# Performance work log

Measured on AMD Instinct MI355X. Metric: run time of the kernel, lower is better.

Reference implementation:

```python
import jax, jax.numpy as jnp
import numpy as np
import math

DIM = 2048
NH = 16
Q_RANK = 1536
KV_RANK = 512
D_NOPE = 128
D_ROPE = 64
D_V = 128
EPS = 1e-6
B, S = 2, 2048
THETA = 10000.0


def _rms_norm(x, w):
    return x * jax.lax.rsqrt(jnp.mean(x * x, axis=-1, keepdims=True) + EPS) * w


def _rope_cos_sin(seq_len, d):
    inv_freq = 1.0 / (THETA ** (jnp.arange(0, d, 2, dtype=jnp.float32) / d))
    t = jnp.arange(seq_len, dtype=jnp.float32)
    freqs = jnp.outer(t, inv_freq)  # (s, d/2)
    return jnp.cos(freqs), jnp.sin(freqs)


def _apply_rope(x, cos, sin):
    # x: (b, s, h, d), rotate interleaved pairs (llama-style complex rotation)
    x1 = x[..., 0::2]
    x2 = x[..., 1::2]
    c = cos[None, :, None, :]
    s = sin[None, :, None, :]
    o1 = x1 * c - x2 * s
    o2 = x1 * s + x2 * c
    return jnp.stack([o1, o2], axis=-1).reshape(x.shape)


def setup_inputs() -> dict:
    key = jax.random.key(0)
    ks = jax.random.split(key, 10)
    sd = 0.02
    return {
        "x": jax.random.normal(ks[0], (B, S, DIM), dtype=jnp.float32),
        # torch nn.Linear weights: (out_features, in_features), y = x @ W.T
        "wq_down": jax.random.normal(ks[1], (Q_RANK, DIM), dtype=jnp.float32) * sd,
        "wq_up": jax.random.normal(ks[2], (NH * D_NOPE, Q_RANK), dtype=jnp.float32) * sd,
        "wq_rope": jax.random.normal(ks[3], (NH * D_ROPE, Q_RANK), dtype=jnp.float32) * sd,
        "q_norm_w": jnp.ones((Q_RANK,), dtype=jnp.float32),
        "wkv_down": jax.random.normal(ks[4], (KV_RANK, DIM), dtype=jnp.float32) * sd,
        "kv_norm_w": jnp.ones((KV_RANK,), dtype=jnp.float32),
        "wkv_up": jax.random.normal(ks[5], (NH * (D_NOPE + D_V), KV_RANK), dtype=jnp.float32) * sd,
        "wk_rope": jax.random.normal(ks[6], (D_ROPE, DIM), dtype=jnp.float32) * sd,
        "wo": jax.random.normal(ks[7], (DIM, NH * D_V), dtype=jnp.float32) * sd,
    }


def reference(x, wq_down, wq_up, wq_rope, q_norm_w, wkv_down, kv_norm_w, wkv_up, wk_rope, wo):
    bs, seq_len, _ = x.shape
    # --- Q low-rank path ---
    q_c = _rms_norm(x @ wq_down.T, q_norm_w)                    # (b, s, q_rank)
    q_nope = (q_c @ wq_up.T).reshape(bs, seq_len, NH, D_NOPE)
    q_pe = (q_c @ wq_rope.T).reshape(bs, seq_len, NH, D_ROPE)
    # --- KV low-rank path ---
    kv_c = _rms_norm(x @ wkv_down.T, kv_norm_w)                 # (b, s, kv_rank)
    kv_up = (kv_c @ wkv_up.T).reshape(bs, seq_len, NH, D_NOPE + D_V)
    k_nope = kv_up[..., :D_NOPE]
    v = kv_up[..., D_NOPE:]                                     # (b, s, h, dv)
    # shared single-head rope key
    k_rope_shared = (x @ wk_rope.T).reshape(bs, seq_len, 1, D_ROPE)
    # --- partial-dim RoPE ---
    cos, sin = _rope_cos_sin(seq_len, D_ROPE)
    q_pe = _apply_rope(q_pe, cos, sin)
    k_rope_shared = _apply_rope(k_rope_shared, cos, sin)
    k_rope = jnp.broadcast_to(k_rope_shared, (bs, seq_len, NH, D_ROPE))
    # --- concat nope + rope dims ---
    q = jnp.concatenate([q_nope, q_pe], axis=-1)                # (b, s, h, dn+dr)
    k = jnp.concatenate([k_nope, k_rope], axis=-1)
    scale = 1.0 / math.sqrt(D_NOPE + D_ROPE)
    scores = jnp.einsum("bqhd,bkhd->bhqk", q, k) * scale        # (b, h, s, s)
    causal = jnp.tril(jnp.ones((seq_len, seq_len), dtype=bool))
    scores = jnp.where(causal[None, None], scores, -jnp.inf)
    probs = jax.nn.softmax(scores.astype(jnp.float32), axis=-1).astype(q.dtype)
    out = jnp.einsum("bhqk,bkhd->bqhd", probs, v)               # (b, s, h, dv)
    out = out.reshape(bs, seq_len, NH * D_V)
    return out @ wo.T


if __name__ == "__main__":
    inp = setup_inputs()
    y = jax.jit(reference)(**inp)
    print(y.shape, y.dtype)
```

## Files before the change

kernel.cpp:

```cpp
#include <hip/hip_runtime.h>
#include <hip/hip_bf16.h>
#include <math.h>

#define NHH 16
#define SS  2048
#define TT  4096
#define DQK 192
#define QSCALE 0.07216878364870322f
#define ROPE_C 0.28782313662425574f

typedef __bf16 bf16x8 __attribute__((ext_vector_type(8)));
typedef float f32x4 __attribute__((ext_vector_type(4)));

#define GLOAD16(gp, lp) __builtin_amdgcn_global_load_lds( \
    (const __attribute__((address_space(1))) void*)(gp),  \
    (__attribute__((address_space(3))) void*)(lp), 16, 0, 0)

#define SEG0 8388608
#define SEG1 11534336
#define SEG2 12582912
#define SEG3 12713984
#define SEG4 15859712
#define SEG5 17432576
#define SEG6 19529728
#define SEG7 23724032

__global__ __launch_bounds__(256) void cast_all(
        const float* __restrict__ x, const float* __restrict__ wqd,
        const float* __restrict__ wkvd, const float* __restrict__ wkr,
        const float* __restrict__ wqu, const float* __restrict__ wqr,
        const float* __restrict__ wkvu, const float* __restrict__ wo,
        __bf16* __restrict__ xb, __bf16* __restrict__ wqd_b,
        __bf16* __restrict__ wkvd_b, __bf16* __restrict__ wkr_b,
        __bf16* __restrict__ wqu_b, __bf16* __restrict__ wqr_b,
        __bf16* __restrict__ wkvu_b, __bf16* __restrict__ wo_b) {
    const int i = (blockIdx.x * 256 + threadIdx.x) * 8;
    const float* src;
    __bf16* dst;
    int off;
    if (i < SEG0)      { src = x;    dst = xb;     off = i; }
    else if (i < SEG1) { src = wqd;  dst = wqd_b;  off = i - SEG0; }
    else if (i < SEG2) { src = wkvd; dst = wkvd_b; off = i - SEG1; }
    else if (i < SEG3) { src = wkr;  dst = wkr_b;  off = i - SEG2; }
    else if (i < SEG4) { src = wqu;  dst = wqu_b;  off = i - SEG3; }
    else if (i < SEG5) { src = wqr;  dst = wqr_b;  off = i - SEG4; }
    else if (i < SEG6) { src = wkvu; dst = wkvu_b; off = i - SEG5; }
    else               { src = wo;   dst = wo_b;   off = i - SEG6; }
    const float4 a = *(const float4*)(src + off);
    const float4 b = *(const float4*)(src + off + 4);
    __bf16 o[8] = {(__bf16)a.x, (__bf16)a.y, (__bf16)a.z, (__bf16)a.w,
                   (__bf16)b.x, (__bf16)b.y, (__bf16)b.z, (__bf16)b.w};
    *(bf16x8*)(dst + off) = *(const bf16x8*)o;
}

__global__ __launch_bounds__(256) void rmsnorm_k(const float* __restrict__ in,
                                                 __bf16* __restrict__ out,
                                                 const float* __restrict__ w, int N) {
    const int row = blockIdx.x;
    const float* xr = in + (size_t)row * N;
    float ss = 0.f;
    for (int i = threadIdx.x; i < N; i += 256) {
        float v = xr[i];
        ss += v * v;
    }
    __shared__ float red[256];
    red[threadIdx.x] = ss;
    __syncthreads();
    for (int s = 128; s > 0; s >>= 1) {
        if (threadIdx.x < s) red[threadIdx.x] += red[threadIdx.x + s];
        __syncthreads();
    }
    const float scale = rsqrtf(red[0] / (float)N + 1e-6f);
    __bf16* orow = out + (size_t)row * N;
    for (int i = threadIdx.x; i < N; i += 256) orow[i] = (__bf16)(xr[i] * scale * w[i]);
}

template<int MODE>
__global__ __launch_bounds__(512, 1) void gemm9(
        const __bf16* __restrict__ A,
        const __bf16* __restrict__ W0, const __bf16* __restrict__ W1,
        const __bf16* __restrict__ W2,
        float* __restrict__ F0, float* __restrict__ F1,
        __bf16* __restrict__ B0, __bf16* __restrict__ B1,
        int M, int N, int Kin) {
    __shared__ __bf16 lds[3 * 24576];
    const int tid = threadIdx.x;
    const int w = tid >> 6, l = tid & 63;
    const int lr = l & 15, lg = l >> 4;
    const int wm = w >> 2, wn = w & 3;

    int m0, n0, nlim = 256, K = Kin;
    bool isKV = false;
    const __bf16* Ause = A;
    if (MODE == 0) {
        const int fb = blockIdx.x;
        if (fb < 256) { m0 = (fb >> 3) * 128; n0 = (fb & 7) * 256; }
        else          { m0 = (fb - 256) * 128; n0 = 2048; }
        nlim = 2112 - n0;
    } else if (MODE == 1) {
        int fb = blockIdx.x;
        isKV = (fb >= 384);
        if (isKV) { fb -= 384; K = 512; Ause = (const __bf16*)F0; }
        m0 = (fb & 31) * 128;
        n0 = (fb >> 5) * 256;
    } else {
        m0 = blockIdx.y * 128; n0 = blockIdx.x * 256;
    }
    const bool fullB = (nlim >= 256);
    const bool wAct  = (wn * 64 < nlim);

    const int srow = (w << 3) + (l >> 3);
    const int scol = (l & 7) << 3;
    const int sswz = ((srow >> 1) & 7) << 3;
    const int csw  = scol ^ sswz;

    const __bf16* aptr[2];
#pragma unroll
    for (int a = 0; a < 2; ++a)
        aptr[a] = Ause + (size_t)(m0 + a * 64 + srow) * K + csw;

    const __bf16* bptr[4];
#pragma unroll
    for (int bb = 0; bb < 4; ++bb) {
        const int n = n0 + bb * 64 + srow;
        const __bf16* wp;
        if (MODE == 0) {
            if (n < 1536)      wp = W0 + (size_t)n * K;
            else if (n < 2048) wp = W1 + (size_t)(n - 1536) * K;
            else if (n < 2112) wp = W2 + (size_t)(n - 2048) * K;
            else               wp = W0;
        } else if (MODE == 1) {
            if (isKV)          wp = W2 + (size_t)n * K;
            else               wp = (n < 2048) ? W0 + (size_t)n * K
                                               : W1 + (size_t)(n - 2048) * K;
        } else {
            wp = W0 + (size_t)n * K;
        }
        bptr[bb] = wp + csw;
    }

    auto stA = [&](int t2, int a) {
        GLOAD16(aptr[a] + (size_t)t2 * 64,
                &lds[(t2 % 3) * 24576 + a * 4096 + tid * 8]);
    };
    auto stB = [&](int t2, int b) {
        GLOAD16(bptr[b] + (size_t)t2 * 64,
                &lds[(t2 % 3) * 24576 + 8192 + b * 4096 + tid * 8]);
    };

    const int rswz = ((lr >> 1) & 7) << 3;

    f32x4 acc[4][4];
#pragma unroll
    for (int i = 0; i < 4; ++i)
#pragma unroll
        for (int j = 0; j < 4; ++j) acc[i][j] = (f32x4){0.f, 0.f, 0.f, 0.f};

    const int NT = K >> 6;
#pragma unroll
    for (int t = 0; t < 2; ++t) {
        stA(t, 0); stA(t, 1);
        stB(t, 0);
        if (fullB) { stB(t, 1); stB(t, 2); stB(t, 3); }
    }

    for (int t = 0; t < NT; ++t) {
        if (t + 1 < NT) {
            if (fullB) asm volatile("s_waitcnt vmcnt(6)" ::: "memory");
            else       asm volatile("s_waitcnt vmcnt(3)" ::: "memory");
        } else {
            asm volatile("s_waitcnt vmcnt(0)" ::: "memory");
        }
        __builtin_amdgcn_s_barrier();

        const __bf16* As_ = &lds[(t % 3) * 24576];
        const __bf16* Bs_ = As_ + 8192;

        if (t + 2 < NT) {
            const int t2 = t + 2;
            stA(t2, 0); stA(t2, 1);
            stB(t2, 0);
            if (fullB) { stB(t2, 1); stB(t2, 2); stB(t2, 3); }
        }

        if (wAct) {
            bf16x8 fa[4][2], fb[4][2];
#pragma unroll
            for (int i = 0; i < 4; ++i)
#pragma unroll
                for (int kk = 0; kk < 2; ++kk)
                    fa[i][kk] = *(const bf16x8*)&As_[(wm * 64 + i * 16 + lr) * 64 +
                                                     ((kk * 32 + lg * 8) ^ rswz)];
#pragma unroll
            for (int j = 0; j < 4; ++j)
#pragma unroll
                for (int kk = 0; kk < 2; ++kk)
                    fb[j][kk] = *(const bf16x8*)&Bs_[(wn * 64 + j * 16 + lr) * 64 +
                                                     ((kk * 32 + lg * 8) ^ rswz)];
            __builtin_amdgcn_s_setprio(1);
#pragma unroll
            for (int i = 0; i < 4; ++i)
#pragma unroll
                for (int j = 0; j < 4; ++j)
#pragma unroll
                    for (int kk = 0; kk < 2; ++kk)
                        acc[i][j] = __builtin_amdgcn_mfma_f32_16x16x32_bf16(fa[i][kk], fb[j][kk], acc[i][j], 0, 0, 0);
            __builtin_amdgcn_s_setprio(0);
        }
    }

    if (!wAct) return;

#pragma unroll
    for (int i = 0; i < 4; ++i) {
#pragma unroll
        for (int j = 0; j < 4; ++j) {
#pragma unroll
            for (int r = 0; r < 4; ++r) {
                const int m = m0 + wm * 64 + i * 16 + lg * 4 + r;
                const int n = n0 + wn * 64 + j * 16 + lr;
                const float v = acc[i][j][r];
                float vp = 0.f;
                if (MODE == 0 || MODE == 1) vp = __shfl_xor(v, 1);
                if (MODE == 0) {
                    if (n < 1536) {
                        F0[(size_t)m * 1536 + n] = v;
                    } else if (n < 2048) {
                        F1[(size_t)m * 512 + (n - 1536)] = v;
                    } else if (n < 2112) {
                        const int jj = n - 2048;
                        const int fi = jj >> 1;
                        const int spos = m & (SS - 1);
                        const float freq = __expf(-ROPE_C * (float)fi);
                        const float ang = (float)spos * freq;
                        const float sn = __sinf(ang), cs = __cosf(ang);
                        const float o = (jj & 1) ? (vp * sn + v * cs) : (v * cs - vp * sn);
                        B0[(size_t)m * 64 + jj] = (__bf16)o;
                    }
                } else if (MODE == 1) {
                    if (!isKV) {
                        if (n < 2048) {
                            B0[(size_t)m * 3072 + (n >> 7) * 192 + (n & 127)] = (__bf16)(v * QSCALE);
                        } else {
                            const int jj = n - 2048;
                            const int h = jj >> 6, dd = jj & 63;
                            const int fi = dd >> 1;
                            const int spos = m & (SS - 1);
                            const float freq = __expf(-ROPE_C * (float)fi);
                            const float ang = (float)spos * freq;
                            const float sn = __sinf(ang), cs = __cosf(ang);
                            const float o = (dd & 1) ? (vp * sn + v * cs) : (v * cs - vp * sn);
                            B0[(size_t)m * 3072 + h * 192 + 128 + dd] = (__bf16)(o * QSCALE);
                        }
                    } else {
                        __bf16* vTo = (__bf16*)F1;
                        const int h = n >> 8, off = n & 255;
                        if (off < 128)
                            B1[(size_t)m * 2048 + h * 128 + off] = (__bf16)v;
                        else
                            vTo[(((size_t)(m >> 11) * NHH + h) * 128 + (off - 128)) * SS + (m & (SS - 1))] = (__bf16)v;
                    }
                } else {
                    F0[(size_t)m * N + n] = v;
                }
            }
        }
    }
}

__global__ __launch_bounds__(512, 1) void attn_mfma7(
        const __bf16* __restrict__ q, const __bf16* __restrict__ knope,
        const __bf16* __restrict__ krope, const __bf16* __restrict__ vT,
        __bf16* __restrict__ att) {
    const int flat = blockIdx.x;
    const int xcd = flat & 7;
    const int a0 = flat >> 3;
    const int bx = a0 & 7;
    const int g8 = ((a0 >> 3) << 3) | xcd;
    const int h = g8 & 15;
    const int b = g8 >> 4;

    const int tid = threadIdx.x;
    const int w  = tid >> 6;
    const int l  = tid & 63;
    const int lr = l & 15;
    const int lg = l >> 4;

    __shared__ __bf16 Ks[2][64][200];
    __shared__ __bf16 Vs[2][128][72];
    __shared__ __bf16 Ps[8][2][16][72];

    const int rg[2] = {bx * 128 + w * 16, (15 - bx) * 128 + w * 16};
    const int nkt = 2 * (15 - bx) + 2;

    bf16x8 sreg[5];
    auto stage_load = [&](int kv0) {
#pragma unroll
        for (int i = 0; i < 5; ++i) {
            const int gc = tid + 512 * i;
            if (gc < 1536) {
                const int row = gc / 24, cc = gc - row * 24;
                const size_t tt = (size_t)(b * SS + kv0 + row);
                const __bf16* src = (cc < 16)
                    ? knope + tt * 2048 + h * 128 + cc * 8
                    : krope + tt * 64 + (cc - 16) * 8;
                sreg[i] = *(const bf16x8*)src;
            } else {
                const int c = gc - 1536;
                const int row = c >> 3, cc = c & 7;
                sreg[i] = *(const bf16x8*)(vT + (((size_t)b * NHH + h) * 128 + row) * SS
                                              + kv0 + cc * 8);
            }
        }
    };
    auto stage_write = [&](int bi) {
#pragma unroll
        for (int i = 0; i < 5; ++i) {
            const int gc = tid + 512 * i;
            if (gc < 1536) {
                const int row = gc / 24, cc = gc - row * 24;
                *(bf16x8*)&Ks[bi][row][cc * 8] = sreg[i];
            } else {
                const int c = gc - 1536;
                *(bf16x8*)&Vs[bi][c >> 3][(c & 7) * 8] = sreg[i];
            }
        }
    };

    bf16x8 qf[2][6];
#pragma unroll
    for (int grp = 0; grp < 2; ++grp) {
        const __bf16* qb = q + (((size_t)(b * SS + rg[grp] + lr)) * NHH + h) * DQK + lg * 8;
#pragma unroll
        for (int c = 0; c < 6; ++c) qf[grp][c] = *(const bf16x8*)(qb + c * 32);
    }

    f32x4 O[2][8];
    float m_r[2][4], l_r[2][4];
#pragma unroll
    for (int grp = 0; grp < 2; ++grp) {
#pragma unroll
        for (int n = 0; n < 8; ++n) O[grp][n] = (f32x4){0.f, 0.f, 0.f, 0.f};
#pragma unroll
        for (int r = 0; r < 4; ++r) { m_r[grp][r] = -INFINITY; l_r[grp][r] = 0.f; }
    }

    stage_load(0);
    stage_write(0);
    __syncthreads();
    int cur = 0;

    for (int kt = 0; kt < nkt; ++kt) {
        const int kv0 = kt * 64;
        const bool hasNext = (kt + 1 < nkt);
        if (hasNext) stage_load(kv0 + 64);

        const bool act0 = kv0 <= rg[0] + 15;
        const bool act1 = kv0 <= rg[1] + 15;
        if (act1 || act0) {
            f32x4 sc[2][4];
#pragma unroll
            for (int s = 0; s < 4; ++s) {
                const int colb = kv0 + s * 16;
                if (colb <= rg[1] + 15 || colb <= rg[0] + 15) {
                    bf16x8 kf[6];
#pragma unroll
                    for (int c = 0; c < 6; ++c)
                        kf[c] = *(const bf16x8*)&Ks[cur][s * 16 + lr][c * 32 + lg * 8];
                    __builtin_amdgcn_s_setprio(1);
#pragma unroll
                    for (int grp = 0; grp < 2; ++grp) {
                        if (colb <= rg[grp] + 15) {
                            f32x4 acc = (f32x4){0.f, 0.f, 0.f, 0.f};
#pragma unroll
                            for (int c = 0; c < 6; ++c)
                                acc = __builtin_amdgcn_mfma_f32_16x16x32_bf16(qf[grp][c], kf[c], acc, 0, 0, 0);
                            sc[grp][s] = acc;
                        } else {
                            sc[grp][s] = (f32x4){-INFINITY, -INFINITY, -INFINITY, -INFINITY};
                        }
                    }
                    __builtin_amdgcn_s_setprio(0);
                } else {
                    sc[0][s] = (f32x4){-INFINITY, -INFINITY, -INFINITY, -INFINITY};
                    sc[1][s] = (f32x4){-INFINITY, -INFINITY, -INFINITY, -INFINITY};
                }
            }

#pragma unroll
            for (int grp = 0; grp < 2; ++grp) {
                const bool act = (grp == 0) ? act0 : act1;
                if (!act) continue;
                const int rgg = rg[grp];
#pragma unroll
                for (int s = 0; s < 4; ++s) {
                    const int col = kv0 + s * 16 + lr;
#pragma unroll
                    for (int r = 0; r < 4; ++r)
                        if (col > rgg + lg * 4 + r) sc[grp][s][r] = -INFINITY;
                }
                float mt[4];
#pragma unroll
                for (int r = 0; r < 4; ++r) {
                    float m = fmaxf(fmaxf(sc[grp][0][r], sc[grp][1][r]),
                                    fmaxf(sc[grp][2][r], sc[grp][3][r]));
                    m = fmaxf(m, __shfl_xor(m, 1));
                    m = fmaxf(m, __shfl_xor(m, 2));
                    m = fmaxf(m, __shfl_xor(m, 4));
                    m = fmaxf(m, __shfl_xor(m, 8));
                    mt[r] = m;
                }
                const bool ok = (mt[0] <= m_r[grp][0] + 8.f) && (mt[1] <= m_r[grp][1] + 8.f) &&
                                (mt[2] <= m_r[grp][2] + 8.f) && (mt[3] <= m_r[grp][3] + 8.f);
                if (!__all(ok)) {
#pragma unroll
                    for (int r = 0; r < 4; ++r) {
                        const float mn = fmaxf(m_r[grp][r], mt[r]);
                        const float al = __expf(m_r[grp][r] - mn);
                        m_r[grp][r] = mn;
                        l_r[grp][r] *= al;
#pragma unroll
                        for (int n = 0; n < 8; ++n) O[grp][n][r] *= al;
                    }
                }
#pragma unroll
                for (int s = 0; s < 4; ++s) {
#pragma unroll
                    for (int r = 0; r < 4; ++r) {
                        const float pv = __expf(sc[grp][s][r] - m_r[grp][r]);
                        sc[grp][s][r] = pv;
                        Ps[w][grp][lg * 4 + r][s * 16 + lr] = (__bf16)pv;
                    }
                }
#pragma unroll
                for (int r = 0; r < 4; ++r) {
                    float ls = (sc[grp][0][r] + sc[grp][1][r]) + (sc[grp][2][r] + sc[grp][3][r]);
                    ls += __shfl_xor(ls, 1);
                    ls += __shfl_xor(ls, 2);
                    ls += __shfl_xor(ls, 4);
                    ls += __shfl_xor(ls, 8);
                    l_r[grp][r] += ls;
                }
            }

            bf16x8 pf[2][2];
#pragma unroll
            for (int grp = 0; grp < 2; ++grp)
#pragma unroll
                for (int ks = 0; ks < 2; ++ks)
                    pf[grp][ks] = *(const bf16x8*)&Ps[w][grp][lr][ks * 32 + lg * 8];
#pragma unroll
            for (int n = 0; n < 8; ++n) {
                bf16x8 v0 = *(const bf16x8*)&Vs[cur][n * 16 + lr][lg * 8];
                bf16x8 v1 = *(const bf16x8*)&Vs[cur][n * 16 + lr][32 + lg * 8];
                __builtin_amdgcn_s_setprio(1);
                if (act0) {
                    O[0][n] = __builtin_amdgcn_mfma_f32_16x16x32_bf16(pf[0][0], v0, O[0][n], 0, 0, 0);
                    O[0][n] = __builtin_amdgcn_mfma_f32_16x16x32_bf16(pf[0][1], v1, O[0][n], 0, 0, 0);
                }
                if (act1) {
                    O[1][n] = __builtin_amdgcn_mfma_f32_16x16x32_bf16(pf[1][0], v0, O[1][n], 0, 0, 0);
                    O[1][n] = __builtin_amdgcn_mfma_f32_16x16x32_bf16(pf[1][1], v1, O[1][n], 0, 0, 0);
                }
                __builtin_amdgcn_s_setprio(0);
            }
        }

        if (hasNext) stage_write(cur ^ 1);
        __syncthreads();
        cur ^= 1;
    }

#pragma unroll
    for (int grp = 0; grp < 2; ++grp) {
        float inv[4];
#pragma unroll
        for (int r = 0; r < 4; ++r) inv[r] = 1.0f / l_r[grp][r];
#pragma unroll
        for (int n = 0; n < 8; ++n) {
#pragma unroll
            for (int r = 0; r < 4; ++r) {
                const size_t tt = (size_t)(b * SS + rg[grp] + lg * 4 + r);
                att[(tt * NHH + h) * 128 + n * 16 + lr] = (__bf16)(O[grp][n][r] * inv[r]);
            }
        }
    }
}

extern "C" void kernel_launch(void* const* d_in, const int* in_sizes, int n_in,
                              void* d_out, int out_size, void* d_ws, size_t ws_size,
                              hipStream_t stream) {
    (void)in_sizes; (void)n_in; (void)out_size; (void)ws_size;
    const float* x        = (const float*)d_in[0];
    const float* wq_down  = (const float*)d_in[1];
    const float* wq_up    = (const float*)d_in[2];
    const float* wq_rope  = (const float*)d_in[3];
    const float* q_norm_w = (const float*)d_in[4];
    const float* wkv_down = (const float*)d_in[5];
    const float* kv_norm_w= (const float*)d_in[6];
    const float* wkv_up   = (const float*)d_in[7];
    const float* wk_rope  = (const float*)d_in[8];
    const float* wo       = (const float*)d_in[9];
    float* out = (float*)d_out;

    char* ws = (char*)d_ws;
    float*  q_c   = (float*)(ws + 0);
    __bf16* att   = (__bf16*)(ws + 0);
    float*  kv_c  = (float*)(ws + 25165824);
    __bf16* xb    = (__bf16*)(ws + 33554432);
    __bf16* vT    = (__bf16*)(ws + 33554432);
    __bf16* qc_b  = (__bf16*)(ws + 50331648);
    __bf16* kvc_b = (__bf16*)(ws + 62914560);
    __bf16* krope = (__bf16*)(ws + 67108864);
    __bf16* qbuf  = (__bf16*)(ws + 67633152);
    __bf16* wqd_b = (__bf16*)(ws + 92798976);
    __bf16* wqu_b = (__bf16*)(ws + 99090432);
    __bf16* wqr_b = (__bf16*)(ws + 105381888);
    __bf16* wkvd_b= (__bf16*)(ws + 108527616);
    __bf16* wkvu_b= (__bf16*)(ws + 110624768);
    __bf16* wkr_b = (__bf16*)(ws + 114819072);
    __bf16* wo_b  = (__bf16*)(ws + 115081216);
    __bf16* knope = (__bf16*)d_out;

    const dim3 blk(256);

    cast_all<<<dim3(SEG7 / 2048), blk, 0, stream>>>(
        x, wq_down, wkv_down, wk_rope, wq_up, wq_rope, wkv_up, wo,
        xb, wqd_b, wkvd_b, wkr_b, wqu_b, wqr_b, wkvu_b, wo_b);

    gemm9<0><<<dim3(288), dim3(512), 0, stream>>>(xb, wqd_b, wkvd_b, wkr_b,
                                                  q_c, kv_c, krope, nullptr, TT, 2112, 2048);

    rmsnorm_k<<<dim3(TT), blk, 0, stream>>>(q_c, qc_b, q_norm_w, 1536);
    rmsnorm_k<<<dim3(TT), blk, 0, stream>>>(kv_c, kvc_b, kv_norm_w, 512);

    gemm9<1><<<dim3(896), dim3(512), 0, stream>>>(qc_b, wqu_b, wqr_b, wkvu_b,
                                                  (float*)kvc_b, (float*)vT,
                                                  qbuf, knope, TT, 3072, 1536);

    attn_mfma7<<<dim3(256), dim3(512), 0, stream>>>(qbuf, knope, krope, vT, att);

    gemm9<3><<<dim3(8, 32), dim3(512), 0, stream>>>(att, wo_b, nullptr, nullptr,
                                                    out, nullptr, nullptr, nullptr, TT, 2048, 2048);
}
```

Before: 354.7 us.

## Halve GEMM K-tile to 32 so two blocks fit per CU

The shared GEMM kernel's K step shrinks from 64 to 32, which halves the triple-buffered LDS footprint. The load mapping, swizzle, wait counts and fragment loads are reworked to match. Launch bounds now ask for two 512-thread blocks per CU so that more waves can hide latency. The cost is twice as many barriers and loop iterations per K, less MFMA work per sync, and register pressure under the tighter launch bound.

```diff
diff --git a/kernel.cpp b/kernel.cpp
--- a/kernel.cpp
+++ b/kernel.cpp
@@ -76,14 +76,14 @@
 }
 
 template<int MODE>
-__global__ __launch_bounds__(512, 1) void gemm9(
+__global__ __launch_bounds__(512, 2) void gemm10(
         const __bf16* __restrict__ A,
         const __bf16* __restrict__ W0, const __bf16* __restrict__ W1,
         const __bf16* __restrict__ W2,
         float* __restrict__ F0, float* __restrict__ F1,
         __bf16* __restrict__ B0, __bf16* __restrict__ B1,
         int M, int N, int Kin) {
-    __shared__ __bf16 lds[3 * 24576];
+    __shared__ __bf16 lds[3 * 12288];
     const int tid = threadIdx.x;
     const int w = tid >> 6, l = tid & 63;
     const int lr = l & 15, lg = l >> 4;
@@ -109,20 +109,17 @@
     const bool fullB = (nlim >= 256);
     const bool wAct  = (wn * 64 < nlim);
 
-    const int srow = (w << 3) + (l >> 3);
-    const int scol = (l & 7) << 3;
-    const int sswz = ((srow >> 1) & 7) << 3;
-    const int csw  = scol ^ sswz;
-
-    const __bf16* aptr[2];
-#pragma unroll
-    for (int a = 0; a < 2; ++a)
-        aptr[a] = Ause + (size_t)(m0 + a * 64 + srow) * K + csw;
-
-    const __bf16* bptr[4];
-#pragma unroll
-    for (int bb = 0; bb < 4; ++bb) {
-        const int n = n0 + bb * 64 + srow;
+    const int srow = tid >> 2;
+    const int scol = (tid & 3) << 3;
+    const int csw  = scol ^ (((srow >> 1) & 3) << 3);
+
+    const __bf16* aptr = Ause + (size_t)(m0 + srow) * K + csw;
+
+    const __bf16* bptr[2];
+#pragma unroll
+    for (int i = 0; i < 2; ++i) {
+        const int row = i * 128 + srow;
+        const int n = n0 + row;
         const __bf16* wp;
         if (MODE == 0) {
             if (n < 1536)      wp = W0 + (size_t)n * K;
@@ -136,19 +133,18 @@
         } else {
             wp = W0 + (size_t)n * K;
         }
-        bptr[bb] = wp + csw;
-    }
-
-    auto stA = [&](int t2, int a) {
-        GLOAD16(aptr[a] + (size_t)t2 * 64,
-                &lds[(t2 % 3) * 24576 + a * 4096 + tid * 8]);
+        bptr[i] = wp + csw;
+    }
+
+    auto stA = [&](int t2) {
+        GLOAD16(aptr + (size_t)t2 * 32, &lds[(t2 % 3) * 12288 + tid * 8]);
     };
-    auto stB = [&](int t2, int b) {
-        GLOAD16(bptr[b] + (size_t)t2 * 64,
-                &lds[(t2 % 3) * 24576 + 8192 + b * 4096 + tid * 8]);
+    auto stB = [&](int t2, int i) {
+        GLOAD16(bptr[i] + (size_t)t2 * 32,
+                &lds[(t2 % 3) * 12288 + 4096 + i * 4096 + tid * 8]);
     };
 
-    const int rswz = ((lr >> 1) & 7) << 3;
+    const int rswz = ((lr >> 1) & 3) << 3;
 
     f32x4 acc[4][4];
 #pragma unroll
@@ -156,55 +152,42 @@
 #pragma unroll
         for (int j = 0; j < 4; ++j) acc[i][j] = (f32x4){0.f, 0.f, 0.f, 0.f};
 
-    const int NT = K >> 6;
-#pragma unroll
-    for (int t = 0; t < 2; ++t) {
-        stA(t, 0); stA(t, 1);
-        stB(t, 0);
-        if (fullB) { stB(t, 1); stB(t, 2); stB(t, 3); }
-    }
+    const int NT = K >> 5;
+    stA(0); stB(0, 0); if (fullB) stB(0, 1);
+    stA(1); stB(1, 0); if (fullB) stB(1, 1);
 
     for (int t = 0; t < NT; ++t) {
         if (t + 1 < NT) {
-            if (fullB) asm volatile("s_waitcnt vmcnt(6)" ::: "memory");
-            else       asm volatile("s_waitcnt vmcnt(3)" ::: "memory");
+            if (fullB) asm volatile("s_waitcnt vmcnt(3)" ::: "memory");
+            else       asm volatile("s_waitcnt vmcnt(2)" ::: "memory");
         } else {
             asm volatile("s_waitcnt vmcnt(0)" ::: "memory");
         }
         __builtin_amdgcn_s_barrier();
 
-        const __bf16* As_ = &lds[(t % 3) * 24576];
-        const __bf16* Bs_ = As_ + 8192;
+        const __bf16* As_ = &lds[(t % 3) * 12288];
+        const __bf16* Bs_ = As_ + 4096;
 
         if (t + 2 < NT) {
-            const int t2 = t + 2;
-            stA(t2, 0); stA(t2, 1);
-            stB(t2, 0);
-            if (fullB) { stB(t2, 1); stB(t2, 2); stB(t2, 3); }
+            stA(t + 2); stB(t + 2, 0); if (fullB) stB(t + 2, 1);
         }
 
         if (wAct) {
-            bf16x8 fa[4][2], fb[4][2];
+            bf16x8 fa[4], fb[4];
 #pragma unroll
             for (int i = 0; i < 4; ++i)
-#pragma unroll
-                for (int kk = 0; kk < 2; ++kk)
-                    fa[i][kk] = *(const bf16x8*)&As_[(wm * 64 + i * 16 + lr) * 64 +
-                                                     ((kk * 32 + lg * 8) ^ rswz)];
+                fa[i] = *(const bf16x8*)&As_[(wm * 64 + i * 16 + lr) * 32 +
+                                             ((lg * 8) ^ rswz)];
 #pragma unroll
             for (int j = 0; j < 4; ++j)
-#pragma unroll
-                for (int kk = 0; kk < 2; ++kk)
-                    fb[j][kk] = *(const bf16x8*)&Bs_[(wn * 64 + j * 16 + lr) * 64 +
-                                                     ((kk * 32 + lg * 8) ^ rswz)];
+                fb[j] = *(const bf16x8*)&Bs_[(wn * 64 + j * 16 + lr) * 32 +
+                                             ((lg * 8) ^ rswz)];
             __builtin_amdgcn_s_setprio(1);
 #pragma unroll
             for (int i = 0; i < 4; ++i)
 #pragma unroll
                 for (int j = 0; j < 4; ++j)
-#pragma unroll
-                    for (int kk = 0; kk < 2; ++kk)
-                        acc[i][j] = __builtin_amdgcn_mfma_f32_16x16x32_bf16(fa[i][kk], fb[j][kk], acc[i][j], 0, 0, 0);
+                    acc[i][j] = __builtin_amdgcn_mfma_f32_16x16x32_bf16(fa[i], fb[j], acc[i][j], 0, 0, 0);
             __builtin_amdgcn_s_setprio(0);
         }
     }
@@ -528,18 +511,18 @@
         x, wq_down, wkv_down, wk_rope, wq_up, wq_rope, wkv_up, wo,
         xb, wqd_b, wkvd_b, wkr_b, wqu_b, wqr_b, wkvu_b, wo_b);
 
-    gemm9<0><<<dim3(288), dim3(512), 0, stream>>>(xb, wqd_b, wkvd_b, wkr_b,
-                                                  q_c, kv_c, krope, nullptr, TT, 2112, 2048);
+    gemm10<0><<<dim3(288), dim3(512), 0, stream>>>(xb, wqd_b, wkvd_b, wkr_b,
+                                                   q_c, kv_c, krope, nullptr, TT, 2112, 2048);
 
     rmsnorm_k<<<dim3(TT), blk, 0, stream>>>(q_c, qc_b, q_norm_w, 1536);
     rmsnorm_k<<<dim3(TT), blk, 0, stream>>>(kv_c, kvc_b, kv_norm_w, 512);
 
-    gemm9<1><<<dim3(896), dim3(512), 0, stream>>>(qc_b, wqu_b, wqr_b, wkvu_b,
-                                                  (float*)kvc_b, (float*)vT,
-                                                  qbuf, knope, TT, 3072, 1536);
+    gemm10<1><<<dim3(896), dim3(512), 0, stream>>>(qc_b, wqu_b, wqr_b, wkvu_b,
+                                                   (float*)kvc_b, (float*)vT,
+                                                   qbuf, knope, TT, 3072, 1536);
 
     attn_mfma7<<<dim3(256), dim3(512), 0, stream>>>(qbuf, knope, krope, vT, att);
 
-    gemm9<3><<<dim3(8, 32), dim3(512), 0, stream>>>(att, wo_b, nullptr, nullptr,
-                                                    out, nullptr, nullptr, nullptr, TT, 2048, 2048);
+    gemm10<3><<<dim3(8, 32), dim3(512), 0, stream>>>(att, wo_b, nullptr, nullptr,
+                                                     out, nullptr, nullptr, nullptr, TT, 2048, 2048);
 }
```

New measurement: 322.1 us. 9.2% less time.
